# Kernel optimization log

Hardware: AMD Instinct MI355X
Metric: run time of the kernel (lower is better)

The kernel has to match this reference:

```python
import jax, jax.numpy as jnp
import numpy as np

D_MODEL = 512
D_FFN = 2048
N_LAYERS = 6
VOCAB = 1000
D_STATE = 16
D_CONV = 4
D_INNER = 2 * D_MODEL  # expand=2
DT_RANK = 32           # ceil(d_model/16)
B, LT, LS = 2, 512, 512


def _pos_encoding(length, d_model):
    pos = np.arange(length, dtype=np.float32)[:, None]
    div = np.exp(np.arange(0, d_model, 2, dtype=np.float32) * (-np.log(10000.0) / d_model))
    pe = np.zeros((length, d_model), np.float32)
    pe[:, 0::2] = np.sin(pos * div)
    pe[:, 1::2] = np.cos(pos * div)
    return jnp.asarray(pe)


def _layer_norm(x, g, b, eps=1e-6):
    m = x.mean(-1, keepdims=True)
    v = ((x - m) ** 2).mean(-1, keepdims=True)
    return (x - m) * jax.lax.rsqrt(v + eps) * g + b


def _mamba(x, in_w, conv_w, conv_b, xproj_w, dt_w, dt_b, A_log, Dskip, out_w):
    # x: (b, l, d_model)
    b, l, _ = x.shape
    xz = x @ in_w.T                                   # (b, l, 2*d_inner)
    xc, z = jnp.split(xz, 2, axis=-1)
    # causal depthwise conv over time
    xt = jnp.transpose(xc, (0, 2, 1))                 # (b, d_inner, l)
    xt = jnp.pad(xt, ((0, 0), (0, 0), (D_CONV - 1, 0)))
    xt = jax.lax.conv_general_dilated(
        xt, conv_w, window_strides=(1,), padding='VALID',
        feature_group_count=D_INNER, dimension_numbers=('NCH', 'OIH', 'NCH'))
    xc = jax.nn.silu(jnp.transpose(xt, (0, 2, 1)) + conv_b)  # (b, l, d_inner)
    dbl = xc @ xproj_w.T                              # (b, l, dt_rank + 2*n)
    dt, Bm, Cm = jnp.split(dbl, [DT_RANK, DT_RANK + D_STATE], axis=-1)
    dt = jax.nn.softplus(dt @ dt_w.T + dt_b)          # (b, l, d_inner)
    A = -jnp.exp(A_log)                               # (d_inner, n)

    def step(h, xs):
        dt_t, B_t, C_t, u_t = xs                      # (b,d),(b,n),(b,n),(b,d)
        dA = jnp.exp(dt_t[..., None] * A)             # (b, d, n)
        h = dA * h + (dt_t * u_t)[..., None] * B_t[:, None, :]
        y = jnp.einsum('bdn,bn->bd', h, C_t)
        return h, y

    h0 = jnp.zeros((b, D_INNER, D_STATE), x.dtype)
    xs = (jnp.swapaxes(dt, 0, 1), jnp.swapaxes(Bm, 0, 1),
          jnp.swapaxes(Cm, 0, 1), jnp.swapaxes(xc, 0, 1))
    _, ys = jax.lax.scan(step, h0, xs)                # ys: (l, b, d_inner)
    y = jnp.swapaxes(ys, 0, 1) + xc * Dskip
    y = y * jax.nn.silu(z)
    return y @ out_w.T                                # (b, l, d_model)


def setup_inputs() -> dict:
    key = jax.random.key(0)
    ks = iter(jax.random.split(key, 40))

    def rn(shape, s=0.02):
        return jax.random.normal(next(ks), shape, jnp.float32) * s

    def mamba_params():
        return dict(
            in_w=rn((N_LAYERS, 2 * D_INNER, D_MODEL)),
            conv_w=rn((N_LAYERS, D_INNER, 1, D_CONV), 0.1),
            conv_b=rn((N_LAYERS, D_INNER)),
            xproj=rn((N_LAYERS, DT_RANK + 2 * D_STATE, D_INNER)),
            dtw=rn((N_LAYERS, D_INNER, DT_RANK)),
            dtb=rn((N_LAYERS, D_INNER)),
            Alog=jnp.log(jnp.broadcast_to(jnp.arange(1.0, D_STATE + 1.0, dtype=jnp.float32), (N_LAYERS, D_INNER, D_STATE))),
            D=jnp.ones((N_LAYERS, D_INNER), jnp.float32),
            outw=rn((N_LAYERS, D_MODEL, D_INNER)),
        )

    ps, pc = mamba_params(), mamba_params()
    inp = {
        'src': jax.random.normal(next(ks), (B, LS, D_MODEL), jnp.float32),
        'tgt': jax.random.randint(next(ks), (B, LT), 0, VOCAB),
        'emb': rn((VOCAB, D_MODEL)),
        'in_w_s': ps['in_w'], 'conv_w_s': ps['conv_w'], 'conv_b_s': ps['conv_b'],
        'xproj_s': ps['xproj'], 'dtw_s': ps['dtw'], 'dtb_s': ps['dtb'],
        'Alog_s': ps['Alog'], 'D_s': ps['D'], 'outw_s': ps['outw'],
        'in_w_c': pc['in_w'], 'conv_w_c': pc['conv_w'], 'conv_b_c': pc['conv_b'],
        'xproj_c': pc['xproj'], 'dtw_c': pc['dtw'], 'dtb_c': pc['dtb'],
        'Alog_c': pc['Alog'], 'D_c': pc['D'], 'outw_c': pc['outw'],
        'ffn_w1': rn((N_LAYERS, D_FFN, D_MODEL)),
        'ffn_b1': jnp.zeros((N_LAYERS, D_FFN), jnp.float32),
        'ffn_w2': rn((N_LAYERS, D_MODEL, D_FFN)),
        'ffn_b2': jnp.zeros((N_LAYERS, D_MODEL), jnp.float32),
        'ln_g': jnp.ones((N_LAYERS, 3, D_MODEL), jnp.float32),
        'ln_b': jnp.zeros((N_LAYERS, 3, D_MODEL), jnp.float32),
        'fin_g': jnp.ones((D_MODEL,), jnp.float32),
        'fin_b': jnp.zeros((D_MODEL,), jnp.float32),
    }
    return inp


def reference(src, tgt, emb, in_w_s, conv_w_s, conv_b_s, xproj_s, dtw_s, dtb_s,
              Alog_s, D_s, outw_s, in_w_c, conv_w_c, conv_b_c, xproj_c, dtw_c,
              dtb_c, Alog_c, D_c, outw_c, ffn_w1, ffn_b1, ffn_w2, ffn_b2,
              ln_g, ln_b, fin_g, fin_b):
    # NormalizedEmbedding + sinusoidal positional encoding
    x = emb[tgt] * jnp.sqrt(jnp.asarray(D_MODEL, jnp.float32))
    x = x + _pos_encoding(LT, D_MODEL)[None]
    for i in range(N_LAYERS):
        # self mamba (post-norm, normalize_before=False)
        t2 = _mamba(x, in_w_s[i], conv_w_s[i], conv_b_s[i], xproj_s[i],
                    dtw_s[i], dtb_s[i], Alog_s[i], D_s[i], outw_s[i])
        x = _layer_norm(x + t2, ln_g[i, 0], ln_b[i, 0])
        # cross mamba over concat([memory, tgt]) then take last LT steps
        cat = jnp.concatenate([src, x], axis=1)
        t2 = _mamba(cat, in_w_c[i], conv_w_c[i], conv_b_c[i], xproj_c[i],
                    dtw_c[i], dtb_c[i], Alog_c[i], D_c[i], outw_c[i])[:, -LT:]
        x = _layer_norm(x + t2, ln_g[i, 1], ln_b[i, 1])
        # positionwise FFN
        h = jax.nn.relu(x @ ffn_w1[i].T + ffn_b1[i]) @ ffn_w2[i].T + ffn_b2[i]
        x = _layer_norm(x + h, ln_g[i, 2], ln_b[i, 2])
    return _layer_norm(x, fin_g, fin_b)
```

## Files before the change

### kernel.cpp

```cpp
#include <hip/hip_runtime.h>
#include <math.h>

#define DMODEL 512
#define DINNER 1024
#define DSTATE 16
#define DTRANK 32
#define NLAYERS 6
#define BB 2
#define LT 512
#define LS 512

typedef __attribute__((ext_vector_type(8))) short bf16x8;
typedef __attribute__((ext_vector_type(8))) unsigned short u16x8;
typedef __attribute__((ext_vector_type(4))) float f32x4;

__device__ __forceinline__ unsigned short f2bf(float f) {
  unsigned u = __float_as_uint(f);
  u += 0x7fffu + ((u >> 16) & 1u);
  return (unsigned short)(u >> 16);
}
__device__ __forceinline__ float bf2f(unsigned short u) {
  return __uint_as_float((unsigned)u << 16);
}

template<int EPI>
__device__ __forceinline__ float epi_apply(float acc, float b) {
  if (EPI == 1) { float v = acc + b; return v > 0.f ? v : 0.f; }
  if (EPI == 2) { return acc + b; }
  if (EPI == 3) { float v = acc + b; return fmaxf(v, 0.f) + log1pf(__expf(-fabsf(v))); }
  return acc;
}

__global__ __launch_bounds__(256) void cvt_all_kernel(
    const float* __restrict__ i0, const float* __restrict__ i1,
    const float* __restrict__ i2, const float* __restrict__ i3,
    const float* __restrict__ i4, const float* __restrict__ i5,
    const float* __restrict__ i6, const float* __restrict__ i7,
    const float* __restrict__ i8, const float* __restrict__ i9,
    unsigned short* __restrict__ outbase) {
  int i = blockIdx.x * 256 + threadIdx.x;
  if (i >= 4079616) return;
  const float* in; int off;
  if      (i <  786432) { in = i0; off = i; }
  else if (i < 1572864) { in = i1; off = i -  786432; }
  else if (i < 1622016) { in = i2; off = i - 1572864; }
  else if (i < 1671168) { in = i3; off = i - 1622016; }
  else if (i < 1695744) { in = i4; off = i - 1671168; }
  else if (i < 1720320) { in = i5; off = i - 1695744; }
  else if (i < 2113536) { in = i6; off = i - 1720320; }
  else if (i < 2506752) { in = i7; off = i - 2113536; }
  else if (i < 3293184) { in = i8; off = i - 2506752; }
  else                  { in = i9; off = i - 3293184; }
  float4 a = ((const float4*)in)[off * 2];
  float4 b = ((const float4*)in)[off * 2 + 1];
  u16x8 o;
  o[0] = f2bf(a.x); o[1] = f2bf(a.y); o[2] = f2bf(a.z); o[3] = f2bf(a.w);
  o[4] = f2bf(b.x); o[5] = f2bf(b.y); o[6] = f2bf(b.z); o[7] = f2bf(b.w);
  *(u16x8*)&outbase[(size_t)i * 8] = o;
}

__global__ __launch_bounds__(256) void embed_kernel(const int* __restrict__ tgt,
    const float* __restrict__ emb, float* __restrict__ X,
    unsigned short* __restrict__ Xb) {
  int i = blockIdx.x * 256 + threadIdx.x;
  int d = i & (DMODEL - 1);
  int bt = i >> 9;
  int t = bt & (LT - 1);
  int tok = tgt[bt];
  float div = __expf((float)(d & ~1) * (-9.210340371976184f / (float)DMODEL));
  float ang = (float)t * div;
  float pe = (d & 1) ? cosf(ang) : sinf(ang);
  float v = emb[(size_t)tok * DMODEL + d] * 22.627416997969522f + pe;
  X[i] = v;
  Xb[i] = f2bf(v);
}

__global__ __launch_bounds__(256) void catsrc_kernel(const float* __restrict__ src,
    unsigned short* __restrict__ CATb) {
  int i = blockIdx.x * 256 + threadIdx.x;
  int c8 = (i & 63) * 8;
  int r = i >> 6;
  int b = r >> 9, l = r & 511;
  const float* s = src + ((size_t)b * 512 + l) * DMODEL + c8;
  float4 a = *(const float4*)s;
  float4 bq = *(const float4*)(s + 4);
  u16x8 o;
  o[0] = f2bf(a.x); o[1] = f2bf(a.y); o[2] = f2bf(a.z); o[3] = f2bf(a.w);
  o[4] = f2bf(bq.x); o[5] = f2bf(bq.y); o[6] = f2bf(bq.z); o[7] = f2bf(bq.w);
  *(u16x8*)&CATb[((size_t)b * 1024 + l) * DMODEL + c8] = o;
}

template<int BK, int EPI, bool SPLIT, bool OUTB>
__global__ __launch_bounds__(256) void mgemmA(
    const unsigned short* __restrict__ A, const unsigned short* __restrict__ Bw,
    const float* __restrict__ bias, float* __restrict__ C,
    unsigned short* __restrict__ Cb, int M, int N, int K, int lda) {
  constexpr int PAD = BK + 8;
  constexpr int CHA = BK / 32;
  constexpr int CHB = BK / 16;
  __shared__ __align__(16) unsigned short As[64 * PAD];
  __shared__ __align__(16) unsigned short Bs[128 * PAD];
  const int tid = threadIdx.x;
  const int bn = blockIdx.x * 128;
  const int bm = blockIdx.y * 64;
  const int lane = tid & 63;
  const int w = tid >> 6;
  const int wr = (w >> 1) * 32;
  const int wc = (w & 1) * 64;
  const int l15 = lane & 15;
  const int l4 = lane >> 4;
  const int koff = l4 * 8;
  int kcnt = K, kbeg = 0;
  if (SPLIT) { kcnt = K / (int)gridDim.z; kbeg = blockIdx.z * kcnt; }
  const int nt = kcnt / BK;
  f32x4 acc[2][4] = {};

  int arow_[CHA], ak8_[CHA];
  const unsigned short* Ap[CHA];
#pragma unroll
  for (int i = 0; i < CHA; ++i) {
    int f = tid + 256 * i;
    arow_[i] = f / (BK / 8);
    ak8_[i] = (f % (BK / 8)) * 8;
    Ap[i] = A + (size_t)(bm + arow_[i]) * lda + kbeg + ak8_[i];
  }
  int brow_[CHB], bk8_[CHB];
  const unsigned short* Bp[CHB];
#pragma unroll
  for (int i = 0; i < CHB; ++i) {
    int f = tid + 256 * i;
    brow_[i] = f / (BK / 8);
    bk8_[i] = (f % (BK / 8)) * 8;
    Bp[i] = Bw + (size_t)(bn + brow_[i]) * K + kbeg + bk8_[i];
  }

  u16x8 av[CHA], bv[CHB];
#pragma unroll
  for (int i = 0; i < CHA; ++i) av[i] = *(const u16x8*)Ap[i];
#pragma unroll
  for (int i = 0; i < CHB; ++i) bv[i] = *(const u16x8*)Bp[i];

  for (int t = 0; t < nt; ++t) {
    __syncthreads();
#pragma unroll
    for (int i = 0; i < CHA; ++i) *(u16x8*)&As[arow_[i] * PAD + ak8_[i]] = av[i];
#pragma unroll
    for (int i = 0; i < CHB; ++i) *(u16x8*)&Bs[brow_[i] * PAD + bk8_[i]] = bv[i];
    if (t + 1 < nt) {
      int ko = (t + 1) * BK;
#pragma unroll
      for (int i = 0; i < CHA; ++i) av[i] = *(const u16x8*)(Ap[i] + ko);
#pragma unroll
      for (int i = 0; i < CHB; ++i) bv[i] = *(const u16x8*)(Bp[i] + ko);
    }
    __syncthreads();
#pragma unroll
    for (int kk = 0; kk < BK / 32; ++kk) {
      bf16x8 afr[2], bfr[4];
#pragma unroll
      for (int i = 0; i < 2; ++i)
        afr[i] = *(const bf16x8*)&As[(wr + i * 16 + l15) * PAD + kk * 32 + koff];
#pragma unroll
      for (int j = 0; j < 4; ++j)
        bfr[j] = *(const bf16x8*)&Bs[(wc + j * 16 + l15) * PAD + kk * 32 + koff];
#pragma unroll
      for (int fr = 0; fr < 2; ++fr)
#pragma unroll
        for (int fc = 0; fc < 4; ++fc)
          acc[fr][fc] = __builtin_amdgcn_mfma_f32_16x16x32_bf16(
              afr[fr], bfr[fc], acc[fr][fc], 0, 0, 0);
    }
  }

  if (SPLIT) {
    float* Pz = C + (size_t)blockIdx.z * M * N;
#pragma unroll
    for (int fc = 0; fc < 4; ++fc) {
      int col = bn + wc + fc * 16 + l15;
#pragma unroll
      for (int fr = 0; fr < 2; ++fr) {
        int row0 = bm + wr + fr * 16 + l4 * 4;
#pragma unroll
        for (int r = 0; r < 4; ++r)
          Pz[(size_t)(row0 + r) * N + col] = acc[fr][fc][r];
      }
    }
  } else {
#pragma unroll
    for (int fc = 0; fc < 4; ++fc) {
      int col = bn + wc + fc * 16 + l15;
      float bvs = (EPI != 0) ? bias[col] : 0.f;
#pragma unroll
      for (int fr = 0; fr < 2; ++fr) {
        int row0 = bm + wr + fr * 16 + l4 * 4;
#pragma unroll
        for (int r = 0; r < 4; ++r) {
          float v = epi_apply<EPI>(acc[fr][fc][r], bvs);
          if (OUTB) Cb[(size_t)(row0 + r) * N + col] = f2bf(v);
          else      C[(size_t)(row0 + r) * N + col] = v;
        }
      }
    }
  }
}

template<int BK, int EPI, bool SPLIT, bool OUTB>
__global__ __launch_bounds__(256) void mgemm(
    const unsigned short* __restrict__ A, const unsigned short* __restrict__ Bw,
    const float* __restrict__ bias, float* __restrict__ C,
    unsigned short* __restrict__ Cb, int M, int N, int K, int lda) {
  constexpr int PAD = BK + 8;
  constexpr int CH = BK / 32;
  __shared__ __align__(16) unsigned short As[64 * PAD];
  __shared__ __align__(16) unsigned short Bs[64 * PAD];
  const int tid = threadIdx.x;
  const int bn = blockIdx.x * 64;
  const int bm = blockIdx.y * 64;
  const int lane = tid & 63;
  const int w = tid >> 6;
  const int wr = (w >> 1) * 32;
  const int wc = (w & 1) * 32;
  const int l15 = lane & 15;
  const int l4 = lane >> 4;
  const int koff = l4 * 8;
  int kcnt = K, kbeg = 0;
  if (SPLIT) { kcnt = K / (int)gridDim.z; kbeg = blockIdx.z * kcnt; }
  const int nt = kcnt / BK;
  f32x4 acc[2][2] = {};

  int row_[CH], k8_[CH];
  const unsigned short *Ap[CH], *Bp[CH];
#pragma unroll
  for (int i = 0; i < CH; ++i) {
    int f = tid + 256 * i;
    row_[i] = f / (BK / 8);
    k8_[i] = (f % (BK / 8)) * 8;
    Ap[i] = A + (size_t)(bm + row_[i]) * lda + kbeg + k8_[i];
    Bp[i] = Bw + (size_t)(bn + row_[i]) * K + kbeg + k8_[i];
  }

  u16x8 av[CH], bv[CH];
#pragma unroll
  for (int i = 0; i < CH; ++i) { av[i] = *(const u16x8*)Ap[i]; bv[i] = *(const u16x8*)Bp[i]; }

  for (int t = 0; t < nt; ++t) {
    __syncthreads();
#pragma unroll
    for (int i = 0; i < CH; ++i) {
      *(u16x8*)&As[row_[i] * PAD + k8_[i]] = av[i];
      *(u16x8*)&Bs[row_[i] * PAD + k8_[i]] = bv[i];
    }
    if (t + 1 < nt) {
      int ko = (t + 1) * BK;
#pragma unroll
      for (int i = 0; i < CH; ++i) {
        av[i] = *(const u16x8*)(Ap[i] + ko);
        bv[i] = *(const u16x8*)(Bp[i] + ko);
      }
    }
    __syncthreads();
#pragma unroll
    for (int kk = 0; kk < CH; ++kk) {
      bf16x8 afr[2], bfr[2];
#pragma unroll
      for (int i = 0; i < 2; ++i) {
        afr[i] = *(const bf16x8*)&As[(wr + i * 16 + l15) * PAD + kk * 32 + koff];
        bfr[i] = *(const bf16x8*)&Bs[(wc + i * 16 + l15) * PAD + kk * 32 + koff];
      }
#pragma unroll
      for (int fr = 0; fr < 2; ++fr)
#pragma unroll
        for (int fc = 0; fc < 2; ++fc)
          acc[fr][fc] = __builtin_amdgcn_mfma_f32_16x16x32_bf16(
              afr[fr], bfr[fc], acc[fr][fc], 0, 0, 0);
    }
  }

  if (SPLIT) {
    float* Pz = C + (size_t)blockIdx.z * M * N;
#pragma unroll
    for (int fc = 0; fc < 2; ++fc) {
      int col = bn + wc + fc * 16 + l15;
#pragma unroll
      for (int fr = 0; fr < 2; ++fr) {
        int row0 = bm + wr + fr * 16 + l4 * 4;
#pragma unroll
        for (int r = 0; r < 4; ++r)
          Pz[(size_t)(row0 + r) * N + col] = acc[fr][fc][r];
      }
    }
  } else {
#pragma unroll
    for (int fc = 0; fc < 2; ++fc) {
      int col = bn + wc + fc * 16 + l15;
      float bvs = (EPI != 0) ? bias[col] : 0.f;
#pragma unroll
      for (int fr = 0; fr < 2; ++fr) {
        int row0 = bm + wr + fr * 16 + l4 * 4;
#pragma unroll
        for (int r = 0; r < 4; ++r) {
          float v = epi_apply<EPI>(acc[fr][fc][r], bvs);
          if (OUTB) Cb[(size_t)(row0 + r) * N + col] = f2bf(v);
          else      C[(size_t)(row0 + r) * N + col] = v;
        }
      }
    }
  }
}

__global__ __launch_bounds__(256) void xred_kernel(const float* __restrict__ P,
    unsigned short* __restrict__ DBLb, int total) {
  int i = blockIdx.x * 256 + threadIdx.x;
  if (i >= total) return;
  float s = 0.f;
  for (int z = 0; z < 8; ++z) s += P[(size_t)z * total + i];
  DBLb[i] = f2bf(s);
}

__global__ __launch_bounds__(256) void conv_silu_kernel(
    const unsigned short* __restrict__ xzb, const float* __restrict__ w,
    const float* __restrict__ bias, unsigned short* __restrict__ outb, int L) {
  int idx = blockIdx.x * 256 + threadIdx.x;
  int d = idx & (DINNER - 1);
  int bt = idx >> 10;
  int b = bt / L;
  int t = bt - b * L;
  const unsigned short* col = xzb + ((size_t)b * L) * (2 * DINNER) + d;
  float acc = bias[d];
#pragma unroll
  for (int k = 0; k < 4; ++k) {
    int tt = t - 3 + k;
    if (tt >= 0) acc = fmaf(bf2f(col[(size_t)tt * (2 * DINNER)]), w[d * 4 + k], acc);
  }
  float sig = 1.f / (1.f + __expf(-acc));
  outb[idx] = f2bf(acc * sig);
}

__global__ __launch_bounds__(256) void scan_pass1(
    const unsigned short* __restrict__ dt, const unsigned short* __restrict__ dblb,
    const unsigned short* __restrict__ u, const float* __restrict__ Alog,
    float* __restrict__ P, float* __restrict__ S, int L, int CL) {
  __shared__ float BC[32][32];
  const int tid = threadIdx.x;
  const int d = blockIdx.x * 256 + tid;
  const int b = blockIdx.y;
  const int c = blockIdx.z;
  const int t0 = c * CL;
  if (tid < CL * 4) {
    int t = tid >> 2, j8 = (tid & 3) * 8;
    u16x8 v = *(const u16x8*)(dblb + ((size_t)b * L + t0 + t) * 64 + 32 + j8);
#pragma unroll
    for (int j = 0; j < 8; ++j) BC[t][j8 + j] = bf2f(v[j]);
  }
  float A[16], h[16], Pp[16];
#pragma unroll
  for (int j = 0; j < 4; ++j) {
    float4 a4 = *(const float4*)(Alog + d * 16 + j * 4);
    A[j * 4 + 0] = -__expf(a4.x); A[j * 4 + 1] = -__expf(a4.y);
    A[j * 4 + 2] = -__expf(a4.z); A[j * 4 + 3] = -__expf(a4.w);
  }
#pragma unroll
  for (int n = 0; n < 16; ++n) { h[n] = 0.f; Pp[n] = 1.f; }
  const unsigned short* dtp = dt + ((size_t)b * L + t0) * DINNER + d;
  const unsigned short* up  = u  + ((size_t)b * L + t0) * DINNER + d;
  __syncthreads();
  float dtv = bf2f(dtp[0]), uv = bf2f(up[0]);
  for (int t = 0; t < CL; ++t) {
    float dtn = 0.f, un = 0.f;
    if (t + 1 < CL) {
      dtn = bf2f(dtp[(size_t)(t + 1) * DINNER]);
      un  = bf2f(up[(size_t)(t + 1) * DINNER]);
    }
    float du = dtv * uv;
#pragma unroll
    for (int n = 0; n < 16; ++n) {
      float dA = __expf(dtv * A[n]);
      Pp[n] *= dA;
      h[n] = fmaf(dA, h[n], du * BC[t][n]);
    }
    dtv = dtn; uv = un;
  }
  size_t base = (size_t)c * 32768 + ((size_t)(b * 1024 + d) << 4);
#pragma unroll
  for (int j = 0; j < 4; ++j) {
    *(float4*)&P[base + j * 4] = make_float4(Pp[j*4], Pp[j*4+1], Pp[j*4+2], Pp[j*4+3]);
    *(float4*)&S[base + j * 4] = make_float4(h[j*4], h[j*4+1], h[j*4+2], h[j*4+3]);
  }
}

__global__ __launch_bounds__(256) void scan_pass2(
    const unsigned short* __restrict__ dt, const unsigned short* __restrict__ dblb,
    const unsigned short* __restrict__ u, const unsigned short* __restrict__ xzb,
    const float* __restrict__ Alog, const float* __restrict__ Dsk,
    const float* __restrict__ P, const float* __restrict__ S,
    unsigned short* __restrict__ ysb, int L, int CL, int c0) {
  __shared__ float BC[32][32];
  const int tid = threadIdx.x;
  const int d = blockIdx.x * 256 + tid;
  const int b = blockIdx.y;
  const int c = blockIdx.z + c0;
  const int t0 = c * CL;
  if (tid < CL * 4) {
    int t = tid >> 2, j8 = (tid & 3) * 8;
    u16x8 v = *(const u16x8*)(dblb + ((size_t)b * L + t0 + t) * 64 + 32 + j8);
#pragma unroll
    for (int j = 0; j < 8; ++j) BC[t][j8 + j] = bf2f(v[j]);
  }
  float A[16], h[16];
#pragma unroll
  for (int j = 0; j < 4; ++j) {
    float4 a4 = *(const float4*)(Alog + d * 16 + j * 4);
    A[j * 4 + 0] = -__expf(a4.x); A[j * 4 + 1] = -__expf(a4.y);
    A[j * 4 + 2] = -__expf(a4.z); A[j * 4 + 3] = -__expf(a4.w);
  }
#pragma unroll
  for (int n = 0; n < 16; ++n) h[n] = 0.f;
  size_t sbase = (size_t)(b * 1024 + d) << 4;
  for (int cc = 0; cc < c; ++cc) {
    size_t bb = (size_t)cc * 32768 + sbase;
#pragma unroll
    for (int j = 0; j < 4; ++j) {
      float4 p4 = *(const float4*)&P[bb + j * 4];
      float4 s4 = *(const float4*)&S[bb + j * 4];
      h[j*4+0] = fmaf(p4.x, h[j*4+0], s4.x);
      h[j*4+1] = fmaf(p4.y, h[j*4+1], s4.y);
      h[j*4+2] = fmaf(p4.z, h[j*4+2], s4.z);
      h[j*4+3] = fmaf(p4.w, h[j*4+3], s4.w);
    }
  }
  float Dv = Dsk[d];
  const unsigned short* dtp = dt + ((size_t)b * L + t0) * DINNER + d;
  const unsigned short* up  = u  + ((size_t)b * L + t0) * DINNER + d;
  const unsigned short* zp  = xzb + ((size_t)b * L + t0) * (2 * DINNER) + DINNER + d;
  unsigned short* yp = ysb + ((size_t)(b * 512) + (t0 - c0 * CL)) * DINNER + d;
  __syncthreads();
  float dtv = bf2f(dtp[0]), uv = bf2f(up[0]), zv = bf2f(zp[0]);
  for (int t = 0; t < CL; ++t) {
    float dtn = 0.f, un = 0.f, zn = 0.f;
    if (t + 1 < CL) {
      dtn = bf2f(dtp[(size_t)(t + 1) * DINNER]);
      un  = bf2f(up[(size_t)(t + 1) * DINNER]);
      zn  = bf2f(zp[(size_t)(t + 1) * (2 * DINNER)]);
    }
    float du = dtv * uv;
    float y = 0.f;
#pragma unroll
    for (int n = 0; n < 16; ++n) {
      float dA = __expf(dtv * A[n]);
      h[n] = fmaf(dA, h[n], du * BC[t][n]);
      y = fmaf(h[n], BC[t][16 + n], y);
    }
    float sig = 1.f / (1.f + __expf(-zv));
    yp[(size_t)t * DINNER] = f2bf((y + uv * Dv) * (zv * sig));
    dtv = dtn; uv = un; zv = zn;
  }
}

template<int NZ, int EPI>
__global__ __launch_bounds__(64) void ln_red_kernel(
    const float* __restrict__ res, const float* __restrict__ P,
    const float* __restrict__ bias, const float* __restrict__ g,
    const float* __restrict__ be, float* __restrict__ out,
    unsigned short* __restrict__ outb, int row_scale, int row_off) {
  int r = blockIdx.x;
  int b = r >> 9, t = r & 511;
  int lane = threadIdx.x;
  const float* rp = res + (size_t)r * DMODEL;
  size_t ob = ((size_t)(b * row_scale + row_off + t)) * DMODEL;
  float v[8];
  float s = 0.f, ss = 0.f;
#pragma unroll
  for (int j = 0; j < 8; ++j) {
    int col = lane + j * 64;
    float acc = 0.f;
#pragma unroll
    for (int z = 0; z < NZ; ++z) acc += P[(size_t)z * 524288 + (size_t)r * DMODEL + col];
    float bv = (EPI != 0) ? bias[col] : 0.f;
    float x = rp[col] + epi_apply<EPI>(acc, bv);
    v[j] = x; s += x; ss += x * x;
  }
#pragma unroll
  for (int o = 32; o > 0; o >>= 1) { s += __shfl_xor(s, o); ss += __shfl_xor(ss, o); }
  float m = s * (1.f / 512.f);
  float var = ss * (1.f / 512.f) - m * m;
  float rs = rsqrtf(var + 1e-6f);
#pragma unroll
  for (int j = 0; j < 8; ++j) {
    int col = lane + j * 64;
    float o2 = (v[j] - m) * rs * g[col] + be[col];
    out[(size_t)r * DMODEL + col] = o2;
    outb[ob + col] = f2bf(o2);
  }
}

__global__ __launch_bounds__(64) void ln_final_kernel(
    const float* __restrict__ res, const float* __restrict__ g,
    const float* __restrict__ be, float* __restrict__ out) {
  int r = blockIdx.x;
  int lane = threadIdx.x;
  const float* rp = res + (size_t)r * DMODEL;
  float v[8];
  float s = 0.f, ss = 0.f;
#pragma unroll
  for (int j = 0; j < 8; ++j) {
    float x = rp[lane + j * 64];
    v[j] = x; s += x; ss += x * x;
  }
#pragma unroll
  for (int o = 32; o > 0; o >>= 1) { s += __shfl_xor(s, o); ss += __shfl_xor(ss, o); }
  float m = s * (1.f / 512.f);
  float var = ss * (1.f / 512.f) - m * m;
  float rs = rsqrtf(var + 1e-6f);
#pragma unroll
  for (int j = 0; j < 8; ++j) {
    int c = lane + j * 64;
    out[(size_t)r * DMODEL + c] = (v[j] - m) * rs * g[c] + be[c];
  }
}

extern "C" void kernel_launch(void* const* d_in, const int* in_sizes, int n_in,
                              void* d_out, int out_size, void* d_ws, size_t ws_size,
                              hipStream_t stream) {
  (void)in_sizes; (void)n_in; (void)out_size; (void)ws_size;
  const float* src      = (const float*)d_in[0];
  const int*   tgt      = (const int*)d_in[1];
  const float* emb      = (const float*)d_in[2];
  const float* in_w_s   = (const float*)d_in[3];
  const float* conv_w_s = (const float*)d_in[4];
  const float* conv_b_s = (const float*)d_in[5];
  const float* xproj_s  = (const float*)d_in[6];
  const float* dtw_s    = (const float*)d_in[7];
  const float* dtb_s    = (const float*)d_in[8];
  const float* Alog_s   = (const float*)d_in[9];
  const float* D_s      = (const float*)d_in[10];
  const float* outw_s   = (const float*)d_in[11];
  const float* in_w_c   = (const float*)d_in[12];
  const float* conv_w_c = (const float*)d_in[13];
  const float* conv_b_c = (const float*)d_in[14];
  const float* xproj_c  = (const float*)d_in[15];
  const float* dtw_c    = (const float*)d_in[16];
  const float* dtb_c    = (const float*)d_in[17];
  const float* Alog_c   = (const float*)d_in[18];
  const float* D_c      = (const float*)d_in[19];
  const float* outw_c   = (const float*)d_in[20];
  const float* ffn_w1   = (const float*)d_in[21];
  const float* ffn_b1   = (const float*)d_in[22];
  const float* ffn_w2   = (const float*)d_in[23];
  const float* ffn_b2   = (const float*)d_in[24];
  const float* ln_g     = (const float*)d_in[25];
  const float* ln_b     = (const float*)d_in[26];
  const float* fin_g    = (const float*)d_in[27];
  const float* fin_b    = (const float*)d_in[28];

  float* ws   = (float*)d_ws;
  float* X    = ws;
  float* XZ   = X + 524288;
  float* SC_P = XZ + 4194304;
  float* SC_S = SC_P + 1048576;
  unsigned short* U = (unsigned short*)(SC_S + 1048576);
  unsigned short* Xb   = U;
  unsigned short* CATb = Xb + 524288;
  unsigned short* XCb  = CATb + 1048576;
  unsigned short* DBLb = XCb + 2097152;
  unsigned short* XZb  = DBLb + 131072;
  unsigned short* YSb  = XZb + 4194304;
  unsigned short* DTb  = YSb + 1048576;
  unsigned short* WB   = DTb + 2097152;
  unsigned short* inwsb = WB;
  unsigned short* inwcb = inwsb + 6291456;
  unsigned short* xpsb  = inwcb + 6291456;
  unsigned short* xpcb  = xpsb + 393216;
  unsigned short* dtwsb = xpcb + 393216;
  unsigned short* dtwcb = dtwsb + 196608;
  unsigned short* owsb  = dtwcb + 196608;
  unsigned short* owcb  = owsb + 3145728;
  unsigned short* f1b   = owcb + 3145728;
  unsigned short* f2b   = f1b + 6291456;

  cvt_all_kernel<<<15936, 256, 0, stream>>>(
      in_w_s, in_w_c, xproj_s, xproj_c, dtw_s, dtw_c, outw_s, outw_c,
      ffn_w1, ffn_w2, WB);
  embed_kernel<<<2048, 256, 0, stream>>>(tgt, emb, X, Xb);
  catsrc_kernel<<<256, 256, 0, stream>>>(src, CATb);

  for (int i = 0; i < NLAYERS; ++i) {
    mgemmA<64, 0, false, true><<<dim3(16, 16), 256, 0, stream>>>(
        Xb, inwsb + (size_t)i * 1048576, nullptr, nullptr, XZb, 1024, 2048, 512, 512);
    conv_silu_kernel<<<4096, 256, 0, stream>>>(
        XZb, conv_w_s + (size_t)i * 4096, conv_b_s + (size_t)i * 1024, XCb, 512);
    mgemm<64, 0, true, false><<<dim3(1, 16, 8), 256, 0, stream>>>(
        XCb, xpsb + (size_t)i * 65536, nullptr, SC_P, nullptr, 1024, 64, 1024, 1024);
    xred_kernel<<<256, 256, 0, stream>>>(SC_P, DBLb, 65536);
    mgemm<32, 3, false, true><<<dim3(16, 16), 256, 0, stream>>>(
        DBLb, dtwsb + (size_t)i * 32768, dtb_s + (size_t)i * 1024, nullptr, DTb,
        1024, 1024, 32, 64);
    scan_pass1<<<dim3(4, 2, 32), 256, 0, stream>>>(
        DTb, DBLb, XCb, Alog_s + (size_t)i * 16384, SC_P, SC_S, 512, 16);
    scan_pass2<<<dim3(4, 2, 32), 256, 0, stream>>>(
        DTb, DBLb, XCb, XZb, Alog_s + (size_t)i * 16384, D_s + (size_t)i * 1024,
        SC_P, SC_S, YSb, 512, 16, 0);
    mgemmA<64, 0, true, false><<<dim3(4, 16, 4), 256, 0, stream>>>(
        YSb, owsb + (size_t)i * 524288, nullptr, XZ, nullptr, 1024, 512, 1024, 1024);
    ln_red_kernel<4, 0><<<1024, 64, 0, stream>>>(
        X, XZ, nullptr, ln_g + (size_t)(i * 3 + 0) * 512,
        ln_b + (size_t)(i * 3 + 0) * 512, X, CATb, 1024, 512);

    mgemmA<64, 0, false, true><<<dim3(16, 32), 256, 0, stream>>>(
        CATb, inwcb + (size_t)i * 1048576, nullptr, nullptr, XZb, 2048, 2048, 512, 512);
    conv_silu_kernel<<<8192, 256, 0, stream>>>(
        XZb, conv_w_c + (size_t)i * 4096, conv_b_c + (size_t)i * 1024, XCb, 1024);
    mgemm<64, 0, true, false><<<dim3(1, 32, 8), 256, 0, stream>>>(
        XCb, xpcb + (size_t)i * 65536, nullptr, SC_P, nullptr, 2048, 64, 1024, 1024);
    xred_kernel<<<512, 256, 0, stream>>>(SC_P, DBLb, 131072);
    mgemm<32, 3, false, true><<<dim3(16, 32), 256, 0, stream>>>(
        DBLb, dtwcb + (size_t)i * 32768, dtb_c + (size_t)i * 1024, nullptr, DTb,
        2048, 1024, 32, 64);
    scan_pass1<<<dim3(4, 2, 32), 256, 0, stream>>>(
        DTb, DBLb, XCb, Alog_c + (size_t)i * 16384, SC_P, SC_S, 1024, 32);
    scan_pass2<<<dim3(4, 2, 16), 256, 0, stream>>>(
        DTb, DBLb, XCb, XZb, Alog_c + (size_t)i * 16384, D_c + (size_t)i * 1024,
        SC_P, SC_S, YSb, 1024, 32, 16);
    mgemmA<64, 0, true, false><<<dim3(4, 16, 4), 256, 0, stream>>>(
        YSb, owcb + (size_t)i * 524288, nullptr, XZ, nullptr, 1024, 512, 1024, 1024);
    ln_red_kernel<4, 0><<<1024, 64, 0, stream>>>(
        X, XZ, nullptr, ln_g + (size_t)(i * 3 + 1) * 512,
        ln_b + (size_t)(i * 3 + 1) * 512, X, Xb, 512, 0);

    mgemmA<64, 1, false, true><<<dim3(16, 16), 256, 0, stream>>>(
        Xb, f1b + (size_t)i * 1048576, ffn_b1 + (size_t)i * 2048, nullptr, XZb,
        1024, 2048, 512, 512);
    mgemmA<64, 0, true, false><<<dim3(4, 16, 8), 256, 0, stream>>>(
        XZb, f2b + (size_t)i * 1048576, nullptr, XZ, nullptr, 1024, 512, 2048, 2048);
    ln_red_kernel<8, 2><<<1024, 64, 0, stream>>>(
        X, XZ, ffn_b2 + (size_t)i * 512, ln_g + (size_t)(i * 3 + 2) * 512,
        ln_b + (size_t)(i * 3 + 2) * 512, X, Xb, 512, 0);
  }

  ln_final_kernel<<<1024, 64, 0, stream>>>(X, fin_g, fin_b, (float*)d_out);
}
```

Before: 1.194 ms.

## Fuse x_proj split-K reduction into dt GEMM and scan loads, vectorize conv

Drops the separate xred kernel. The dt-projection GEMM (new mgemm_dt, a single 64x64 MFMA tile with K=32) and both scan passes now sum the 8 split-K partials of x_proj directly from fp32 scratch. This removes a launch and a bf16 round-trip per mamba block, and the scans now read B/C in fp32. The cost is redundant partial-sum reads across dt GEMM column blocks. It also vectorizes the causal conv to 8 channels per thread and changes the weight conversion kernel to 4 elements per thread.

```diff
diff --git a/kernel.cpp b/kernel.cpp
--- a/kernel.cpp
+++ b/kernel.cpp
@@ -39,24 +39,21 @@
     const float* __restrict__ i8, const float* __restrict__ i9,
     unsigned short* __restrict__ outbase) {
   int i = blockIdx.x * 256 + threadIdx.x;
-  if (i >= 4079616) return;
+  if (i >= 8159232) return;
   const float* in; int off;
-  if      (i <  786432) { in = i0; off = i; }
-  else if (i < 1572864) { in = i1; off = i -  786432; }
-  else if (i < 1622016) { in = i2; off = i - 1572864; }
-  else if (i < 1671168) { in = i3; off = i - 1622016; }
-  else if (i < 1695744) { in = i4; off = i - 1671168; }
-  else if (i < 1720320) { in = i5; off = i - 1695744; }
-  else if (i < 2113536) { in = i6; off = i - 1720320; }
-  else if (i < 2506752) { in = i7; off = i - 2113536; }
-  else if (i < 3293184) { in = i8; off = i - 2506752; }
-  else                  { in = i9; off = i - 3293184; }
-  float4 a = ((const float4*)in)[off * 2];
-  float4 b = ((const float4*)in)[off * 2 + 1];
-  u16x8 o;
-  o[0] = f2bf(a.x); o[1] = f2bf(a.y); o[2] = f2bf(a.z); o[3] = f2bf(a.w);
-  o[4] = f2bf(b.x); o[5] = f2bf(b.y); o[6] = f2bf(b.z); o[7] = f2bf(b.w);
-  *(u16x8*)&outbase[(size_t)i * 8] = o;
+  if      (i < 1572864) { in = i0; off = i; }
+  else if (i < 3145728) { in = i1; off = i - 1572864; }
+  else if (i < 3244032) { in = i2; off = i - 3145728; }
+  else if (i < 3342336) { in = i3; off = i - 3244032; }
+  else if (i < 3391488) { in = i4; off = i - 3342336; }
+  else if (i < 3440640) { in = i5; off = i - 3391488; }
+  else if (i < 4227072) { in = i6; off = i - 3440640; }
+  else if (i < 5013504) { in = i7; off = i - 4227072; }
+  else if (i < 6586368) { in = i8; off = i - 5013504; }
+  else                  { in = i9; off = i - 6586368; }
+  float4 a = ((const float4*)in)[off];
+  ushort4 o = make_ushort4(f2bf(a.x), f2bf(a.y), f2bf(a.z), f2bf(a.w));
+  *(ushort4*)&outbase[(size_t)i * 4] = o;
 }
 
 __global__ __launch_bounds__(256) void embed_kernel(const int* __restrict__ tgt,
@@ -308,36 +305,114 @@
   }
 }
 
-__global__ __launch_bounds__(256) void xred_kernel(const float* __restrict__ P,
-    unsigned short* __restrict__ DBLb, int total) {
-  int i = blockIdx.x * 256 + threadIdx.x;
-  if (i >= total) return;
-  float s = 0.f;
-  for (int z = 0; z < 8; ++z) s += P[(size_t)z * total + i];
-  DBLb[i] = f2bf(s);
+__global__ __launch_bounds__(256) void mgemm_dt(
+    const float* __restrict__ XPP, const unsigned short* __restrict__ Bw,
+    const float* __restrict__ bias, unsigned short* __restrict__ Cb,
+    int M, int N) {
+  constexpr int PAD = 40;
+  __shared__ __align__(16) unsigned short As[64 * PAD];
+  __shared__ __align__(16) unsigned short Bs[64 * PAD];
+  const int tid = threadIdx.x;
+  const int bn = blockIdx.x * 64;
+  const int bm = blockIdx.y * 64;
+  const int lane = tid & 63;
+  const int w = tid >> 6;
+  const int wr = (w >> 1) * 32;
+  const int wc = (w & 1) * 32;
+  const int l15 = lane & 15;
+  const int l4 = lane >> 4;
+  const int koff = l4 * 8;
+  const size_t zs = (size_t)M * 64;
+  {
+    int r = tid >> 2, c8 = (tid & 3) * 8;
+    const float* p = XPP + (size_t)(bm + r) * 64 + c8;
+    float s[8] = {0.f, 0.f, 0.f, 0.f, 0.f, 0.f, 0.f, 0.f};
+#pragma unroll
+    for (int z = 0; z < 8; ++z) {
+      float4 a = *(const float4*)(p + z * zs);
+      float4 b = *(const float4*)(p + z * zs + 4);
+      s[0] += a.x; s[1] += a.y; s[2] += a.z; s[3] += a.w;
+      s[4] += b.x; s[5] += b.y; s[6] += b.z; s[7] += b.w;
+    }
+    u16x8 o;
+#pragma unroll
+    for (int j = 0; j < 8; ++j) o[j] = f2bf(s[j]);
+    *(u16x8*)&As[r * PAD + c8] = o;
+    *(u16x8*)&Bs[r * PAD + c8] = *(const u16x8*)(Bw + (size_t)(bn + r) * 32 + c8);
+  }
+  __syncthreads();
+  bf16x8 afr[2], bfr[2];
+#pragma unroll
+  for (int i = 0; i < 2; ++i) {
+    afr[i] = *(const bf16x8*)&As[(wr + i * 16 + l15) * PAD + koff];
+    bfr[i] = *(const bf16x8*)&Bs[(wc + i * 16 + l15) * PAD + koff];
+  }
+  f32x4 acc[2][2] = {};
+#pragma unroll
+  for (int fr = 0; fr < 2; ++fr)
+#pragma unroll
+    for (int fc = 0; fc < 2; ++fc)
+      acc[fr][fc] = __builtin_amdgcn_mfma_f32_16x16x32_bf16(
+          afr[fr], bfr[fc], acc[fr][fc], 0, 0, 0);
+#pragma unroll
+  for (int fc = 0; fc < 2; ++fc) {
+    int col = bn + wc + fc * 16 + l15;
+    float bvs = bias[col];
+#pragma unroll
+    for (int fr = 0; fr < 2; ++fr) {
+      int row0 = bm + wr + fr * 16 + l4 * 4;
+#pragma unroll
+      for (int r = 0; r < 4; ++r)
+        Cb[(size_t)(row0 + r) * N + col] = f2bf(epi_apply<3>(acc[fr][fc][r], bvs));
+    }
+  }
 }
 
 __global__ __launch_bounds__(256) void conv_silu_kernel(
     const unsigned short* __restrict__ xzb, const float* __restrict__ w,
     const float* __restrict__ bias, unsigned short* __restrict__ outb, int L) {
   int idx = blockIdx.x * 256 + threadIdx.x;
-  int d = idx & (DINNER - 1);
-  int bt = idx >> 10;
+  int d8 = (idx & 127) * 8;
+  int bt = idx >> 7;
   int b = bt / L;
   int t = bt - b * L;
-  const unsigned short* col = xzb + ((size_t)b * L) * (2 * DINNER) + d;
-  float acc = bias[d];
+  const unsigned short* col = xzb + ((size_t)b * L) * (2 * DINNER) + d8;
+  float acc[8];
+  float4 wv[8];
+#pragma unroll
+  for (int j = 0; j < 8; ++j) {
+    acc[j] = bias[d8 + j];
+    wv[j] = *(const float4*)(w + (size_t)(d8 + j) * 4);
+  }
 #pragma unroll
   for (int k = 0; k < 4; ++k) {
     int tt = t - 3 + k;
-    if (tt >= 0) acc = fmaf(bf2f(col[(size_t)tt * (2 * DINNER)]), w[d * 4 + k], acc);
-  }
-  float sig = 1.f / (1.f + __expf(-acc));
-  outb[idx] = f2bf(acc * sig);
+    if (tt >= 0) {
+      u16x8 v = *(const u16x8*)(col + (size_t)tt * (2 * DINNER));
+      float wk[8] = {
+        k == 0 ? wv[0].x : k == 1 ? wv[0].y : k == 2 ? wv[0].z : wv[0].w,
+        k == 0 ? wv[1].x : k == 1 ? wv[1].y : k == 2 ? wv[1].z : wv[1].w,
+        k == 0 ? wv[2].x : k == 1 ? wv[2].y : k == 2 ? wv[2].z : wv[2].w,
+        k == 0 ? wv[3].x : k == 1 ? wv[3].y : k == 2 ? wv[3].z : wv[3].w,
+        k == 0 ? wv[4].x : k == 1 ? wv[4].y : k == 2 ? wv[4].z : wv[4].w,
+        k == 0 ? wv[5].x : k == 1 ? wv[5].y : k == 2 ? wv[5].z : wv[5].w,
+        k == 0 ? wv[6].x : k == 1 ? wv[6].y : k == 2 ? wv[6].z : wv[6].w,
+        k == 0 ? wv[7].x : k == 1 ? wv[7].y : k == 2 ? wv[7].z : wv[7].w };
+#pragma unroll
+      for (int j = 0; j < 8; ++j) acc[j] = fmaf(bf2f(v[j]), wk[j], acc[j]);
+    }
+  }
+  u16x8 o;
+#pragma unroll
+  for (int j = 0; j < 8; ++j) {
+    float sig = 1.f / (1.f + __expf(-acc[j]));
+    o[j] = f2bf(acc[j] * sig);
+  }
+  *(u16x8*)&outb[(size_t)bt * DINNER + d8] = o;
 }
 
 __global__ __launch_bounds__(256) void scan_pass1(
-    const unsigned short* __restrict__ dt, const unsigned short* __restrict__ dblb,
+    const unsigned short* __restrict__ dt, const float* __restrict__ XPP,
     const unsigned short* __restrict__ u, const float* __restrict__ Alog,
     float* __restrict__ P, float* __restrict__ S, int L, int CL) {
   __shared__ float BC[32][32];
@@ -348,9 +423,18 @@
   const int t0 = c * CL;
   if (tid < CL * 4) {
     int t = tid >> 2, j8 = (tid & 3) * 8;
-    u16x8 v = *(const u16x8*)(dblb + ((size_t)b * L + t0 + t) * 64 + 32 + j8);
-#pragma unroll
-    for (int j = 0; j < 8; ++j) BC[t][j8 + j] = bf2f(v[j]);
+    const float* p = XPP + ((size_t)b * L + t0 + t) * 64 + 32 + j8;
+    const size_t zs = (size_t)BB * L * 64;
+    float s[8] = {0.f, 0.f, 0.f, 0.f, 0.f, 0.f, 0.f, 0.f};
+#pragma unroll
+    for (int z = 0; z < 8; ++z) {
+      float4 a = *(const float4*)(p + z * zs);
+      float4 bq = *(const float4*)(p + z * zs + 4);
+      s[0] += a.x; s[1] += a.y; s[2] += a.z; s[3] += a.w;
+      s[4] += bq.x; s[5] += bq.y; s[6] += bq.z; s[7] += bq.w;
+    }
+#pragma unroll
+    for (int j = 0; j < 8; ++j) BC[t][j8 + j] = s[j];
   }
   float A[16], h[16], Pp[16];
 #pragma unroll
@@ -389,7 +473,7 @@
 }
 
 __global__ __launch_bounds__(256) void scan_pass2(
-    const unsigned short* __restrict__ dt, const unsigned short* __restrict__ dblb,
+    const unsigned short* __restrict__ dt, const float* __restrict__ XPP,
     const unsigned short* __restrict__ u, const unsigned short* __restrict__ xzb,
     const float* __restrict__ Alog, const float* __restrict__ Dsk,
     const float* __restrict__ P, const float* __restrict__ S,
@@ -402,9 +486,18 @@
   const int t0 = c * CL;
   if (tid < CL * 4) {
     int t = tid >> 2, j8 = (tid & 3) * 8;
-    u16x8 v = *(const u16x8*)(dblb + ((size_t)b * L + t0 + t) * 64 + 32 + j8);
-#pragma unroll
-    for (int j = 0; j < 8; ++j) BC[t][j8 + j] = bf2f(v[j]);
+    const float* p = XPP + ((size_t)b * L + t0 + t) * 64 + 32 + j8;
+    const size_t zs = (size_t)BB * L * 64;
+    float s[8] = {0.f, 0.f, 0.f, 0.f, 0.f, 0.f, 0.f, 0.f};
+#pragma unroll
+    for (int z = 0; z < 8; ++z) {
+      float4 a = *(const float4*)(p + z * zs);
+      float4 bq = *(const float4*)(p + z * zs + 4);
+      s[0] += a.x; s[1] += a.y; s[2] += a.z; s[3] += a.w;
+      s[4] += bq.x; s[5] += bq.y; s[6] += bq.z; s[7] += bq.w;
+    }
+#pragma unroll
+    for (int j = 0; j < 8; ++j) BC[t][j8 + j] = s[j];
   }
   float A[16], h[16];
 #pragma unroll
@@ -555,14 +648,14 @@
   float* ws   = (float*)d_ws;
   float* X    = ws;
   float* XZ   = X + 524288;
-  float* SC_P = XZ + 4194304;
+  float* XPP  = XZ + 4194304;
+  float* SC_P = XPP + 1048576;
   float* SC_S = SC_P + 1048576;
   unsigned short* U = (unsigned short*)(SC_S + 1048576);
   unsigned short* Xb   = U;
   unsigned short* CATb = Xb + 524288;
   unsigned short* XCb  = CATb + 1048576;
-  unsigned short* DBLb = XCb + 2097152;
-  unsigned short* XZb  = DBLb + 131072;
+  unsigned short* XZb  = XCb + 2097152;
   unsigned short* YSb  = XZb + 4194304;
   unsigned short* DTb  = YSb + 1048576;
   unsigned short* WB   = DTb + 2097152;
@@ -577,7 +670,7 @@
   unsigned short* f1b   = owcb + 3145728;
   unsigned short* f2b   = f1b + 6291456;
 
-  cvt_all_kernel<<<15936, 256, 0, stream>>>(
+  cvt_all_kernel<<<31872, 256, 0, stream>>>(
       in_w_s, in_w_c, xproj_s, xproj_c, dtw_s, dtw_c, outw_s, outw_c,
       ffn_w1, ffn_w2, WB);
   embed_kernel<<<2048, 256, 0, stream>>>(tgt, emb, X, Xb);
@@ -586,18 +679,16 @@
   for (int i = 0; i < NLAYERS; ++i) {
     mgemmA<64, 0, false, true><<<dim3(16, 16), 256, 0, stream>>>(
         Xb, inwsb + (size_t)i * 1048576, nullptr, nullptr, XZb, 1024, 2048, 512, 512);
-    conv_silu_kernel<<<4096, 256, 0, stream>>>(
+    conv_silu_kernel<<<512, 256, 0, stream>>>(
         XZb, conv_w_s + (size_t)i * 4096, conv_b_s + (size_t)i * 1024, XCb, 512);
     mgemm<64, 0, true, false><<<dim3(1, 16, 8), 256, 0, stream>>>(
-        XCb, xpsb + (size_t)i * 65536, nullptr, SC_P, nullptr, 1024, 64, 1024, 1024);
-    xred_kernel<<<256, 256, 0, stream>>>(SC_P, DBLb, 65536);
-    mgemm<32, 3, false, true><<<dim3(16, 16), 256, 0, stream>>>(
-        DBLb, dtwsb + (size_t)i * 32768, dtb_s + (size_t)i * 1024, nullptr, DTb,
-        1024, 1024, 32, 64);
+        XCb, xpsb + (size_t)i * 65536, nullptr, XPP, nullptr, 1024, 64, 1024, 1024);
+    mgemm_dt<<<dim3(16, 16), 256, 0, stream>>>(
+        XPP, dtwsb + (size_t)i * 32768, dtb_s + (size_t)i * 1024, DTb, 1024, 1024);
     scan_pass1<<<dim3(4, 2, 32), 256, 0, stream>>>(
-        DTb, DBLb, XCb, Alog_s + (size_t)i * 16384, SC_P, SC_S, 512, 16);
+        DTb, XPP, XCb, Alog_s + (size_t)i * 16384, SC_P, SC_S, 512, 16);
     scan_pass2<<<dim3(4, 2, 32), 256, 0, stream>>>(
-        DTb, DBLb, XCb, XZb, Alog_s + (size_t)i * 16384, D_s + (size_t)i * 1024,
+        DTb, XPP, XCb, XZb, Alog_s + (size_t)i * 16384, D_s + (size_t)i * 1024,
         SC_P, SC_S, YSb, 512, 16, 0);
     mgemmA<64, 0, true, false><<<dim3(4, 16, 4), 256, 0, stream>>>(
         YSb, owsb + (size_t)i * 524288, nullptr, XZ, nullptr, 1024, 512, 1024, 1024);
@@ -607,18 +698,16 @@
 
     mgemmA<64, 0, false, true><<<dim3(16, 32), 256, 0, stream>>>(
         CATb, inwcb + (size_t)i * 1048576, nullptr, nullptr, XZb, 2048, 2048, 512, 512);
-    conv_silu_kernel<<<8192, 256, 0, stream>>>(
+    conv_silu_kernel<<<1024, 256, 0, stream>>>(
         XZb, conv_w_c + (size_t)i * 4096, conv_b_c + (size_t)i * 1024, XCb, 1024);
     mgemm<64, 0, true, false><<<dim3(1, 32, 8), 256, 0, stream>>>(
-        XCb, xpcb + (size_t)i * 65536, nullptr, SC_P, nullptr, 2048, 64, 1024, 1024);
-    xred_kernel<<<512, 256, 0, stream>>>(SC_P, DBLb, 131072);
-    mgemm<32, 3, false, true><<<dim3(16, 32), 256, 0, stream>>>(
-        DBLb, dtwcb + (size_t)i * 32768, dtb_c + (size_t)i * 1024, nullptr, DTb,
-        2048, 1024, 32, 64);
+        XCb, xpcb + (size_t)i * 65536, nullptr, XPP, nullptr, 2048, 64, 1024, 1024);
+    mgemm_dt<<<dim3(16, 32), 256, 0, stream>>>(
+        XPP, dtwcb + (size_t)i * 32768, dtb_c + (size_t)i * 1024, DTb, 2048, 1024);
     scan_pass1<<<dim3(4, 2, 32), 256, 0, stream>>>(
-        DTb, DBLb, XCb, Alog_c + (size_t)i * 16384, SC_P, SC_S, 1024, 32);
+        DTb, XPP, XCb, Alog_c + (size_t)i * 16384, SC_P, SC_S, 1024, 32);
     scan_pass2<<<dim3(4, 2, 16), 256, 0, stream>>>(
-        DTb, DBLb, XCb, XZb, Alog_c + (size_t)i * 16384, D_c + (size_t)i * 1024,
+        DTb, XPP, XCb, XZb, Alog_c + (size_t)i * 16384, D_c + (size_t)i * 1024,
         SC_P, SC_S, YSb, 1024, 32, 16);
     mgemmA<64, 0, true, false><<<dim3(4, 16, 4), 256, 0, stream>>>(
         YSb, owcb + (size_t)i * 524288, nullptr, XZ, nullptr, 1024, 512, 1024, 1024);
```

Measured after the change: 1.194 ms. Within noise of the previous version (+0.0%).
